# Optimization experiments

Hardware: AMD Instinct MI355X
Metric: run time of the kernel (lower is better)

The kernel has to match this reference:

```python
import jax, jax.numpy as jnp
import numpy as np

N_NODES = 100000
N_EDGES = 1000000
IN_DIM = 128
HID = 128
OUT_DIM = 40


def setup_inputs() -> dict:
    key = jax.random.key(0)
    ks = jax.random.split(key, 16)
    x = jax.random.normal(ks[0], (N_NODES, IN_DIM), dtype=jnp.float32)
    edge_index = jax.random.randint(ks[1], (2, N_EDGES), 0, N_NODES, dtype=jnp.int64)
    s = 0.05
    # GAT layer 1 (in->hid, heads=1, concat=True)
    W1 = jax.random.normal(ks[2], (HID, IN_DIM), jnp.float32) * s
    b1 = jnp.zeros((HID,), jnp.float32)
    att1 = jax.random.normal(ks[3], (1, 2 * HID), jnp.float32) * s
    bias1 = jnp.zeros((HID,), jnp.float32)
    # GAT layer 2 (hid->hid)
    W2 = jax.random.normal(ks[4], (HID, HID), jnp.float32) * s
    b2 = jnp.zeros((HID,), jnp.float32)
    att2 = jax.random.normal(ks[5], (1, 2 * HID), jnp.float32) * s
    bias2 = jnp.zeros((HID,), jnp.float32)
    # post_mp: Linear(hid,hid) -> Dropout -> Linear(hid,out)
    Wp1 = jax.random.normal(ks[6], (HID, HID), jnp.float32) * s
    bp1 = jnp.zeros((HID,), jnp.float32)
    Wp2 = jax.random.normal(ks[7], (OUT_DIM, HID), jnp.float32) * s
    bp2 = jnp.zeros((OUT_DIM,), jnp.float32)
    return dict(x=x, edge_index=edge_index, W1=W1, b1=b1, att1=att1, bias1=bias1,
                W2=W2, b2=b2, att2=att2, bias2=bias2,
                Wp1=Wp1, bp1=bp1, Wp2=Wp2, bp2=bp2)


def gat_layer(x, src, dst, W, b, att, bias, n_nodes):
    # x: [N, Fin] -> h: [N, C] (heads=1, concat=True)
    h = x @ W.T + b
    C = h.shape[1]
    att_i, att_j = att[0, :C], att[0, C:]  # split: first half pairs with x_i (dst), second with x_j (src)
    # per-node scalar projections, then gather per edge (avoids [E,2C] concat)
    e = (h @ att_i)[dst] + (h @ att_j)[src]  # [E]
    e = jnp.where(e > 0, e, 0.2 * e)  # leaky_relu(0.2)
    # segment softmax over destination nodes
    m = jax.ops.segment_max(e, dst, num_segments=n_nodes)
    ex = jnp.exp(e - m[dst])
    denom = jax.ops.segment_sum(ex, dst, num_segments=n_nodes)
    alpha = ex / denom[dst]
    out = jax.ops.segment_sum(h[src] * alpha[:, None], dst, num_segments=n_nodes)
    return out + bias


def reference(x, edge_index, W1, b1, att1, bias1, W2, b2, att2, bias2, Wp1, bp1, Wp2, bp2):
    src, dst = edge_index[0], edge_index[1]
    n = x.shape[0]
    h = jax.nn.relu(gat_layer(x, src, dst, W1, b1, att1, bias1, n))  # dropout p=0 -> identity
    h = jax.nn.relu(gat_layer(h, src, dst, W2, b2, att2, bias2, n))
    y = (h @ Wp1.T + bp1) @ Wp2.T + bp2  # post_mp (eval: dropout identity)
    return jax.nn.log_softmax(y, axis=1)
```

## Files before the change

kernel.cpp:

```cpp
#include <hip/hip_runtime.h>

#define N_NODES 100000
#define N_EDGES 1000000
#define HID 128
#define OUT_DIM 40
#define CSR_W 64
#define CUR_STRIDE 16
#define GEMM_TILES 1563
#define G2_TILES 782
#define PROJ_TILES 1563
#define EDGE_BLK 977
#define WC_BLK 21

typedef __attribute__((ext_vector_type(8))) short bf16x8;
typedef __attribute__((ext_vector_type(4))) float f32x4;

__device__ inline unsigned short f2bf(float f) {
    unsigned u = __float_as_uint(f);
    u += 0x7fffu + ((u >> 16) & 1u);
    return (unsigned short)(u >> 16);
}
__device__ inline float bf2f(unsigned short u) {
    return __uint_as_float(((unsigned)u) << 16);
}

__device__ inline float4 ld4(const float* p) { return *(const float4*)p; }
__device__ inline float4 ld4(const unsigned short* p) {
    ushort4 u = *(const ushort4*)p;
    return make_float4(bf2f(u.x), bf2f(u.y), bf2f(u.z), bf2f(u.w));
}

__global__ __launch_bounds__(256) void zero_kernel(float4* __restrict__ p, int n4) {
    int i = blockIdx.x * 256 + threadIdx.x;
    int stride = gridDim.x * 256;
    float4 z = make_float4(0.f, 0.f, 0.f, 0.f);
    for (; i < n4; i += stride) p[i] = z;
}

#define LDA 136
template<typename AT>
__device__ __forceinline__ void gemm_tile_body(
    int tile, const AT* __restrict__ A, const float* __restrict__ W,
    const float* __restrict__ out_bias, const float* __restrict__ in_bias,
    int relu_in, const float* __restrict__ att,
    unsigned short* __restrict__ Cb, float* __restrict__ hi, float* __restrict__ hj,
    int n_rows, unsigned short* As, unsigned short* Ws)
{
    const int t = threadIdx.x;
    const int row0 = tile * 64;

    for (int i = 0; i < 8; i++) {
        int lin = t + i * 256;
        int r = lin >> 5;
        int k = (lin & 31) * 4;
        int gr = row0 + r;
        float4 av = make_float4(0.f, 0.f, 0.f, 0.f);
        if (gr < n_rows) av = ld4(A + (size_t)gr * HID + k);
        if (in_bias) {
            av.x += in_bias[k + 0]; av.y += in_bias[k + 1];
            av.z += in_bias[k + 2]; av.w += in_bias[k + 3];
            if (relu_in) {
                av.x = fmaxf(av.x, 0.f); av.y = fmaxf(av.y, 0.f);
                av.z = fmaxf(av.z, 0.f); av.w = fmaxf(av.w, 0.f);
            }
        }
        ushort4 bv;
        bv.x = f2bf(av.x); bv.y = f2bf(av.y); bv.z = f2bf(av.z); bv.w = f2bf(av.w);
        *(ushort4*)(&As[r * LDA + k]) = bv;
    }
    for (int i = 0; i < 16; i++) {
        int lin = t + i * 256;
        int r = lin >> 5;
        int k = (lin & 31) * 4;
        float4 wv = *(const float4*)(W + (size_t)r * HID + k);
        ushort4 bv;
        bv.x = f2bf(wv.x); bv.y = f2bf(wv.y); bv.z = f2bf(wv.z); bv.w = f2bf(wv.w);
        *(ushort4*)(&Ws[r * LDA + k]) = bv;
    }
    __syncthreads();

    const int wave = t >> 6, lane = t & 63;
    const int lrow = lane & 15, quad = lane >> 4;
    const int wrow = wave * 16;

    f32x4 acc[8];
    #pragma unroll
    for (int ni = 0; ni < 8; ni++) acc[ni] = (f32x4){0.f, 0.f, 0.f, 0.f};

    #pragma unroll
    for (int ks = 0; ks < 4; ks++) {
        const int kb = ks * 32 + quad * 8;
        bf16x8 af = *(bf16x8*)(&As[(wrow + lrow) * LDA + kb]);
        #pragma unroll
        for (int ni = 0; ni < 8; ni++) {
            bf16x8 bfr = *(bf16x8*)(&Ws[(ni * 16 + lrow) * LDA + kb]);
            acc[ni] = __builtin_amdgcn_mfma_f32_16x16x32_bf16(af, bfr, acc[ni], 0, 0, 0);
        }
    }

    float pi[4] = {0.f, 0.f, 0.f, 0.f}, pj[4] = {0.f, 0.f, 0.f, 0.f};
    const int rbase = row0 + wrow + quad * 4;
    #pragma unroll
    for (int ni = 0; ni < 8; ni++) {
        const int col = ni * 16 + lrow;
        const float bo = out_bias[col];
        const float ai = att[col], aj = att[HID + col];
        #pragma unroll
        for (int r = 0; r < 4; r++) {
            float v = acc[ni][r] + bo;
            int gr = rbase + r;
            if (gr < n_rows) Cb[(size_t)gr * HID + col] = f2bf(v);
            pi[r] = fmaf(v, ai, pi[r]);
            pj[r] = fmaf(v, aj, pj[r]);
        }
    }
    #pragma unroll
    for (int o = 1; o < 16; o <<= 1) {
        #pragma unroll
        for (int r = 0; r < 4; r++) {
            pi[r] += __shfl_xor(pi[r], o);
            pj[r] += __shfl_xor(pj[r], o);
        }
    }
    if (lrow == 0) {
        #pragma unroll
        for (int r = 0; r < 4; r++) {
            int gr = rbase + r;
            if (gr < n_rows) { hi[gr] = pi[r]; hj[gr] = pj[r]; }
        }
    }
}

__global__ __launch_bounds__(256) void combined_prep(
    const float* __restrict__ x, const float* __restrict__ W1,
    const float* __restrict__ b1, const float* __restrict__ att1,
    const float* __restrict__ Wp1, const float* __restrict__ bp1,
    const float* __restrict__ Wp2, const float* __restrict__ bp2,
    const int* __restrict__ src, const int* __restrict__ dst,
    unsigned* __restrict__ cursor, int* __restrict__ csr,
    unsigned short* __restrict__ hbuf, float* __restrict__ hi, float* __restrict__ hj,
    float* __restrict__ Wc, float* __restrict__ bc)
{
    __shared__ unsigned short As[64 * LDA];
    __shared__ unsigned short Ws[128 * LDA];
    const int b = blockIdx.x, g = b >> 3, r = b & 7;

    if (r < 3) {
        const int eid = g * 3 + r;
        if (eid >= EDGE_BLK) return;
        int e = eid * 1024 + threadIdx.x;
        #pragma unroll
        for (int j = 0; j < 4; j++, e += 256) {
            if (e < N_EDGES) {
                int d = dst[e], s = src[e];
                unsigned p = atomicAdd(&cursor[d << 4], 1u);
                if (p < CSR_W) __builtin_nontemporal_store(s, &csr[(d << 6) + p]);
            }
        }
        return;
    }
    const int oid = g * 5 + (r - 3);
    if (oid < WC_BLK) {
        int t = oid * 256 + threadIdx.x;
        if (t < OUT_DIM * HID) {
            int o = t >> 7, k = t & 127;
            float s = 0.f;
            for (int j = 0; j < HID; j++) s = fmaf(Wp2[o * HID + j], Wp1[j * HID + k], s);
            Wc[t] = s;
        } else if (t < OUT_DIM * HID + OUT_DIM) {
            int o = t - OUT_DIM * HID;
            float s = bp2[o];
            for (int j = 0; j < HID; j++) s = fmaf(Wp2[o * HID + j], bp1[j], s);
            bc[o] = s;
        }
        return;
    }
    const int tile = oid - WC_BLK;
    if (tile >= GEMM_TILES) return;
    gemm_tile_body<float>(tile, x, W1, b1, nullptr, 0, att1, hbuf, hi, hj, N_NODES, As, Ws);
}

__global__ __launch_bounds__(256) void gemm_mfma_b128(
    const unsigned short* __restrict__ A, const float* __restrict__ W,
    const float* __restrict__ out_bias, const float* __restrict__ in_bias,
    const float* __restrict__ att,
    unsigned short* __restrict__ Cb, float* __restrict__ hi, float* __restrict__ hj,
    int n_rows)
{
    __shared__ unsigned short As[128 * LDA];
    __shared__ unsigned short Ws[128 * LDA];
    const int t = threadIdx.x;
    const int row0 = blockIdx.x * 128;

    for (int i = 0; i < 16; i++) {
        int lin = t + i * 256;
        int r = lin >> 5;
        int k = (lin & 31) * 4;
        int gr = row0 + r;
        float4 av = make_float4(0.f, 0.f, 0.f, 0.f);
        if (gr < n_rows) av = ld4(A + (size_t)gr * HID + k);
        av.x = fmaxf(av.x + in_bias[k + 0], 0.f);
        av.y = fmaxf(av.y + in_bias[k + 1], 0.f);
        av.z = fmaxf(av.z + in_bias[k + 2], 0.f);
        av.w = fmaxf(av.w + in_bias[k + 3], 0.f);
        ushort4 bv;
        bv.x = f2bf(av.x); bv.y = f2bf(av.y); bv.z = f2bf(av.z); bv.w = f2bf(av.w);
        *(ushort4*)(&As[r * LDA + k]) = bv;
    }
    for (int i = 0; i < 16; i++) {
        int lin = t + i * 256;
        int r = lin >> 5;
        int k = (lin & 31) * 4;
        float4 wv = *(const float4*)(W + (size_t)r * HID + k);
        ushort4 bv;
        bv.x = f2bf(wv.x); bv.y = f2bf(wv.y); bv.z = f2bf(wv.z); bv.w = f2bf(wv.w);
        *(ushort4*)(&Ws[r * LDA + k]) = bv;
    }
    __syncthreads();

    const int wave = t >> 6, lane = t & 63;
    const int lrow = lane & 15, quad = lane >> 4;

    f32x4 acc[2][8];
    #pragma unroll
    for (int mt = 0; mt < 2; mt++)
        #pragma unroll
        for (int ni = 0; ni < 8; ni++) acc[mt][ni] = (f32x4){0.f, 0.f, 0.f, 0.f};

    #pragma unroll
    for (int ks = 0; ks < 4; ks++) {
        const int kb = ks * 32 + quad * 8;
        bf16x8 af0 = *(bf16x8*)(&As[(wave * 32 + lrow) * LDA + kb]);
        bf16x8 af1 = *(bf16x8*)(&As[(wave * 32 + 16 + lrow) * LDA + kb]);
        #pragma unroll
        for (int ni = 0; ni < 8; ni++) {
            bf16x8 bfr = *(bf16x8*)(&Ws[(ni * 16 + lrow) * LDA + kb]);
            acc[0][ni] = __builtin_amdgcn_mfma_f32_16x16x32_bf16(af0, bfr, acc[0][ni], 0, 0, 0);
            acc[1][ni] = __builtin_amdgcn_mfma_f32_16x16x32_bf16(af1, bfr, acc[1][ni], 0, 0, 0);
        }
    }

    #pragma unroll
    for (int mt = 0; mt < 2; mt++) {
        float pi[4] = {0.f, 0.f, 0.f, 0.f}, pj[4] = {0.f, 0.f, 0.f, 0.f};
        const int rbase = row0 + wave * 32 + mt * 16 + quad * 4;
        #pragma unroll
        for (int ni = 0; ni < 8; ni++) {
            const int col = ni * 16 + lrow;
            const float bo = out_bias[col];
            const float ai = att[col], aj = att[HID + col];
            #pragma unroll
            for (int r = 0; r < 4; r++) {
                float v = acc[mt][ni][r] + bo;
                int gr = rbase + r;
                if (gr < n_rows) Cb[(size_t)gr * HID + col] = f2bf(v);
                pi[r] = fmaf(v, ai, pi[r]);
                pj[r] = fmaf(v, aj, pj[r]);
            }
        }
        #pragma unroll
        for (int o = 1; o < 16; o <<= 1) {
            #pragma unroll
            for (int r = 0; r < 4; r++) {
                pi[r] += __shfl_xor(pi[r], o);
                pj[r] += __shfl_xor(pj[r], o);
            }
        }
        if (lrow == 0) {
            #pragma unroll
            for (int r = 0; r < 4; r++) {
                int gr = rbase + r;
                if (gr < n_rows) { hi[gr] = pi[r]; hj[gr] = pj[r]; }
            }
        }
    }
}

__global__ __launch_bounds__(256) void fused_gat(
    const unsigned* __restrict__ cursor, const int* __restrict__ csr,
    const unsigned short* __restrict__ hb,
    const float* __restrict__ hi, const float* __restrict__ hj,
    unsigned short* __restrict__ out)
{
    const int wave = threadIdx.x >> 6;
    const int lane = threadIdx.x & 63;
    const int d = blockIdx.x * 4 + wave;
    if (d >= N_NODES) return;
    unsigned deg = cursor[d << 4];
    if (deg > CSR_W) deg = CSR_W;
    const int cnt = (int)deg;
    const float hid = hi[d];
    const int base = d << 6;

    int sv = 0;
    float ev = -INFINITY;
    if (lane < cnt) {
        sv = csr[base + lane];
        float e = hid + hj[sv];
        ev = e > 0.f ? e : 0.2f * e;
    }
    float m = ev;
    #pragma unroll
    for (int o = 32; o; o >>= 1) m = fmaxf(m, __shfl_xor(m, o));
    const float exv = (lane < cnt) ? __expf(ev - m) : 0.f;
    float denom = exv;
    #pragma unroll
    for (int o = 32; o; o >>= 1) denom += __shfl_xor(denom, o);

    float accx = 0.f, accy = 0.f;
    const int co = lane * 2;
    int i = 0;
    for (; i + 4 <= cnt; i += 4) {
        const int s0 = __shfl(sv, i),     s1 = __shfl(sv, i + 1);
        const int s2 = __shfl(sv, i + 2), s3 = __shfl(sv, i + 3);
        const float w0 = __shfl(exv, i),     w1 = __shfl(exv, i + 1);
        const float w2 = __shfl(exv, i + 2), w3 = __shfl(exv, i + 3);
        const ushort2 u0 = *(const ushort2*)(hb + (size_t)s0 * HID + co);
        const ushort2 u1 = *(const ushort2*)(hb + (size_t)s1 * HID + co);
        const ushort2 u2 = *(const ushort2*)(hb + (size_t)s2 * HID + co);
        const ushort2 u3 = *(const ushort2*)(hb + (size_t)s3 * HID + co);
        accx = fmaf(w0, bf2f(u0.x), accx); accy = fmaf(w0, bf2f(u0.y), accy);
        accx = fmaf(w1, bf2f(u1.x), accx); accy = fmaf(w1, bf2f(u1.y), accy);
        accx = fmaf(w2, bf2f(u2.x), accx); accy = fmaf(w2, bf2f(u2.y), accy);
        accx = fmaf(w3, bf2f(u3.x), accx); accy = fmaf(w3, bf2f(u3.y), accy);
    }
    for (; i < cnt; i++) {
        const int s = __shfl(sv, i);
        const float w = __shfl(exv, i);
        const ushort2 u = *(const ushort2*)(hb + (size_t)s * HID + co);
        accx = fmaf(w, bf2f(u.x), accx);
        accy = fmaf(w, bf2f(u.y), accy);
    }
    const float inv = cnt ? 1.f / denom : 0.f;
    ushort2 o2;
    o2.x = f2bf(accx * inv);
    o2.y = f2bf(accy * inv);
    *(ushort2*)(out + (size_t)d * HID + co) = o2;
}

__global__ __launch_bounds__(256) void final_proj_mfma(
    const unsigned short* __restrict__ agg, const float* __restrict__ bias2,
    const float* __restrict__ Wc, const float* __restrict__ bc,
    float* __restrict__ out)
{
    __shared__ unsigned short As[64 * LDA];
    __shared__ unsigned short Ws[48 * LDA];
    const int t = threadIdx.x;
    const int node0 = blockIdx.x * 64;

    for (int i = 0; i < 5; i++) {
        int lin = t + i * 256;
        int r = lin >> 5;
        int k = (lin & 31) * 4;
        float4 wv = *(const float4*)(Wc + (size_t)r * HID + k);
        ushort4 bv;
        bv.x = f2bf(wv.x); bv.y = f2bf(wv.y); bv.z = f2bf(wv.z); bv.w = f2bf(wv.w);
        *(ushort4*)(&Ws[r * LDA + k]) = bv;
    }
    {
        int r = 40 + (t >> 5);
        int k = (t & 31) * 4;
        ushort4 z; z.x = 0; z.y = 0; z.z = 0; z.w = 0;
        *(ushort4*)(&Ws[r * LDA + k]) = z;
    }
    for (int i = 0; i < 8; i++) {
        int lin = t + i * 256;
        int r = lin >> 5;
        int k = (lin & 31) * 4;
        int gr = node0 + r;
        float4 v = make_float4(0.f, 0.f, 0.f, 0.f);
        if (gr < N_NODES) v = ld4(agg + (size_t)gr * HID + k);
        v.x = fmaxf(v.x + bias2[k + 0], 0.f);
        v.y = fmaxf(v.y + bias2[k + 1], 0.f);
        v.z = fmaxf(v.z + bias2[k + 2], 0.f);
        v.w = fmaxf(v.w + bias2[k + 3], 0.f);
        ushort4 bv;
        bv.x = f2bf(v.x); bv.y = f2bf(v.y); bv.z = f2bf(v.z); bv.w = f2bf(v.w);
        *(ushort4*)(&As[r * LDA + k]) = bv;
    }
    __syncthreads();

    const int wave = t >> 6, lane = t & 63;
    const int lrow = lane & 15, quad = lane >> 4;
    const int wrow = wave * 16;

    f32x4 acc[3];
    #pragma unroll
    for (int nt = 0; nt < 3; nt++) acc[nt] = (f32x4){0.f, 0.f, 0.f, 0.f};

    #pragma unroll
    for (int ks = 0; ks < 4; ks++) {
        const int kb = ks * 32 + quad * 8;
        bf16x8 af = *(bf16x8*)(&As[(wrow + lrow) * LDA + kb]);
        #pragma unroll
        for (int nt = 0; nt < 3; nt++) {
            bf16x8 bfr = *(bf16x8*)(&Ws[(nt * 16 + lrow) * LDA + kb]);
            acc[nt] = __builtin_amdgcn_mfma_f32_16x16x32_bf16(af, bfr, acc[nt], 0, 0, 0);
        }
    }

    int cols[3]; float bcv[3]; bool valid[3];
    #pragma unroll
    for (int nt = 0; nt < 3; nt++) {
        cols[nt] = nt * 16 + lrow;
        valid[nt] = cols[nt] < OUT_DIM;
        bcv[nt] = valid[nt] ? bc[cols[nt]] : 0.f;
    }
    const int rbase = node0 + wrow + quad * 4;
    #pragma unroll
    for (int r = 0; r < 4; r++) {
        float v[3];
        float mx = -INFINITY;
        #pragma unroll
        for (int nt = 0; nt < 3; nt++) {
            v[nt] = acc[nt][r] + bcv[nt];
            if (valid[nt]) mx = fmaxf(mx, v[nt]);
        }
        #pragma unroll
        for (int o = 1; o < 16; o <<= 1) mx = fmaxf(mx, __shfl_xor(mx, o));
        float s = 0.f;
        #pragma unroll
        for (int nt = 0; nt < 3; nt++)
            if (valid[nt]) s += __expf(v[nt] - mx);
        #pragma unroll
        for (int o = 1; o < 16; o <<= 1) s += __shfl_xor(s, o);
        const float lse = mx + __logf(s);
        const int node = rbase + r;
        if (node < N_NODES) {
            #pragma unroll
            for (int nt = 0; nt < 3; nt++)
                if (valid[nt]) out[(size_t)node * OUT_DIM + cols[nt]] = v[nt] - lse;
        }
    }
}

extern "C" void kernel_launch(void* const* d_in, const int* in_sizes, int n_in,
                              void* d_out, int out_size, void* d_ws, size_t ws_size,
                              hipStream_t stream)
{
    const float* x     = (const float*)d_in[0];
    const int*   ei    = (const int*)d_in[1];
    const float* W1    = (const float*)d_in[2];
    const float* b1    = (const float*)d_in[3];
    const float* att1  = (const float*)d_in[4];
    const float* bias1 = (const float*)d_in[5];
    const float* W2    = (const float*)d_in[6];
    const float* b2    = (const float*)d_in[7];
    const float* att2  = (const float*)d_in[8];
    const float* bias2 = (const float*)d_in[9];
    const float* Wp1   = (const float*)d_in[10];
    const float* bp1   = (const float*)d_in[11];
    const float* Wp2   = (const float*)d_in[12];
    const float* bp2   = (const float*)d_in[13];
    float* out = (float*)d_out;

    const int* src = ei;
    const int* dst = ei + N_EDGES;

    char* ws = (char*)d_ws;
    unsigned short* hbuf = (unsigned short*)ws;
    unsigned short* aggb = hbuf + (size_t)N_NODES * HID;
    float* hi      = (float*)(aggb + (size_t)N_NODES * HID);
    float* hj      = hi + N_NODES;
    unsigned* cursor = (unsigned*)(hj + N_NODES);
    int* csr       = (int*)(cursor + (size_t)N_NODES * CUR_STRIDE);
    float* Wc      = (float*)(csr + (size_t)N_NODES * CSR_W);
    float* bc      = Wc + OUT_DIM * HID;

    const int prep_blocks = 326 * 8;

    zero_kernel<<<512, 256, 0, stream>>>((float4*)cursor, N_NODES * CUR_STRIDE / 4);

    combined_prep<<<prep_blocks, 256, 0, stream>>>(
        x, W1, b1, att1, Wp1, bp1, Wp2, bp2, src, dst,
        cursor, csr, hbuf, hi, hj, Wc, bc);

    fused_gat<<<N_NODES / 4, 256, 0, stream>>>(cursor, csr, hbuf, hi, hj, aggb);

    gemm_mfma_b128<<<G2_TILES, 256, 0, stream>>>(aggb, W2, b2, bias1, att2, hbuf, hi, hj, N_NODES);
    fused_gat<<<N_NODES / 4, 256, 0, stream>>>(cursor, csr, hbuf, hi, hj, aggb);

    final_proj_mfma<<<PROJ_TILES, 256, 0, stream>>>(aggb, bias2, Wc, bc, out);
}
```

Before: 313.3 us.

## Store node features as per-row scaled FP8 to halve gather traffic

The GEMM epilogues now quantize the transformed node features to FP8 (e4m3) with a per-row absmax scale instead of bf16. The scale is packed alongside the hj attention term as a float2. The GAT aggregation gathers 2 bytes per lane instead of 4 and folds the row scale into the softmax weight. This roughly halves the random-gather bandwidth in both aggregation passes, at the cost of lower feature precision and a possible accuracy-tolerance risk.

```diff
diff --git a/kernel.cpp b/kernel.cpp
--- a/kernel.cpp
+++ b/kernel.cpp
@@ -14,6 +14,7 @@
 
 typedef __attribute__((ext_vector_type(8))) short bf16x8;
 typedef __attribute__((ext_vector_type(4))) float f32x4;
+typedef __attribute__((ext_vector_type(2))) float f32x2;
 
 __device__ inline unsigned short f2bf(float f) {
     unsigned u = __float_as_uint(f);
@@ -22,6 +23,46 @@
 }
 __device__ inline float bf2f(unsigned short u) {
     return __uint_as_float(((unsigned)u) << 16);
+}
+
+#if __has_builtin(__builtin_amdgcn_cvt_pk_f32_fp8) && __has_builtin(__builtin_amdgcn_cvt_pk_fp8_f32)
+#define HAVE_HW_FP8 1
+#endif
+
+__device__ inline f32x2 fp8x2_to_f32(unsigned short u) {
+#ifdef HAVE_HW_FP8
+    return __builtin_amdgcn_cvt_pk_f32_fp8((int)(unsigned)u, false);
+#else
+    f32x2 r;
+    unsigned v0 = u & 0xFF, v1 = (u >> 8) & 0xFF;
+    unsigned m0 = v0 & 0x7F, m1 = v1 & 0x7F;
+    float a0 = (m0 >= 8) ? __uint_as_float((m0 << 20) + 0x3C000000) : (float)m0 * (1.f/512.f);
+    float a1 = (m1 >= 8) ? __uint_as_float((m1 << 20) + 0x3C000000) : (float)m1 * (1.f/512.f);
+    r.x = (v0 & 0x80) ? -a0 : a0;
+    r.y = (v1 & 0x80) ? -a1 : a1;
+    return r;
+#endif
+}
+
+__device__ inline unsigned char f32_to_fp8(float f) {
+#ifdef HAVE_HW_FP8
+    return (unsigned char)(__builtin_amdgcn_cvt_pk_fp8_f32(f, 0.f, 0u, false) & 0xFF);
+#else
+    float a = fabsf(f);
+    unsigned s = (__float_as_uint(f) >> 31) << 7;
+    if (a >= 448.f) return (unsigned char)(s | 0x7E);
+    if (a < 0.015625f) {
+        int q = (int)rintf(a * 512.f);
+        return (unsigned char)(s | q);
+    }
+    unsigned u = __float_as_uint(a);
+    u += 0x7FFFFu + ((u >> 20) & 1u);
+    int be = (int)(u >> 23) - 120;
+    unsigned m = (u >> 20) & 7;
+    if (be >= 16) return (unsigned char)(s | 0x7E);
+    if (be <= 0) { int q = (int)rintf(a * 512.f); return (unsigned char)(s | q); }
+    return (unsigned char)(s | (be << 3) | m);
+#endif
 }
 
 __device__ inline float4 ld4(const float* p) { return *(const float4*)p; }
@@ -43,7 +84,7 @@
     int tile, const AT* __restrict__ A, const float* __restrict__ W,
     const float* __restrict__ out_bias, const float* __restrict__ in_bias,
     int relu_in, const float* __restrict__ att,
-    unsigned short* __restrict__ Cb, float* __restrict__ hi, float* __restrict__ hj,
+    unsigned char* __restrict__ Cb8, float* __restrict__ hi, float2* __restrict__ hjsc,
     int n_rows, unsigned short* As, unsigned short* Ws)
 {
     const int t = threadIdx.x;
@@ -99,6 +140,7 @@
     }
 
     float pi[4] = {0.f, 0.f, 0.f, 0.f}, pj[4] = {0.f, 0.f, 0.f, 0.f};
+    float amax[4] = {0.f, 0.f, 0.f, 0.f};
     const int rbase = row0 + wrow + quad * 4;
     #pragma unroll
     for (int ni = 0; ni < 8; ni++) {
@@ -108,8 +150,7 @@
         #pragma unroll
         for (int r = 0; r < 4; r++) {
             float v = acc[ni][r] + bo;
-            int gr = rbase + r;
-            if (gr < n_rows) Cb[(size_t)gr * HID + col] = f2bf(v);
+            amax[r] = fmaxf(amax[r], fabsf(v));
             pi[r] = fmaf(v, ai, pi[r]);
             pj[r] = fmaf(v, aj, pj[r]);
         }
@@ -118,15 +159,34 @@
     for (int o = 1; o < 16; o <<= 1) {
         #pragma unroll
         for (int r = 0; r < 4; r++) {
+            amax[r] = fmaxf(amax[r], __shfl_xor(amax[r], o));
             pi[r] += __shfl_xor(pi[r], o);
             pj[r] += __shfl_xor(pj[r], o);
         }
     }
-    if (lrow == 0) {
+    float inv[4], scl[4];
+    #pragma unroll
+    for (int r = 0; r < 4; r++) {
+        float a = fmaxf(amax[r], 1e-20f);
+        scl[r] = a * (1.f / 448.f);
+        inv[r] = 448.f / a;
+    }
+    #pragma unroll
+    for (int ni = 0; ni < 8; ni++) {
+        const int col = ni * 16 + lrow;
+        const float bo = out_bias[col];
         #pragma unroll
         for (int r = 0; r < 4; r++) {
             int gr = rbase + r;
-            if (gr < n_rows) { hi[gr] = pi[r]; hj[gr] = pj[r]; }
+            if (gr < n_rows)
+                Cb8[(size_t)gr * HID + col] = f32_to_fp8((acc[ni][r] + bo) * inv[r]);
+        }
+    }
+    if (lrow == 0) {
+        #pragma unroll
+        for (int r = 0; r < 4; r++) {
+            int gr = rbase + r;
+            if (gr < n_rows) { hi[gr] = pi[r]; hjsc[gr] = make_float2(pj[r], scl[r]); }
         }
     }
 }
@@ -138,7 +198,7 @@
     const float* __restrict__ Wp2, const float* __restrict__ bp2,
     const int* __restrict__ src, const int* __restrict__ dst,
     unsigned* __restrict__ cursor, int* __restrict__ csr,
-    unsigned short* __restrict__ hbuf, float* __restrict__ hi, float* __restrict__ hj,
+    unsigned char* __restrict__ hb8, float* __restrict__ hi, float2* __restrict__ hjsc,
     float* __restrict__ Wc, float* __restrict__ bc)
 {
     __shared__ unsigned short As[64 * LDA];
@@ -177,14 +237,14 @@
     }
     const int tile = oid - WC_BLK;
     if (tile >= GEMM_TILES) return;
-    gemm_tile_body<float>(tile, x, W1, b1, nullptr, 0, att1, hbuf, hi, hj, N_NODES, As, Ws);
+    gemm_tile_body<float>(tile, x, W1, b1, nullptr, 0, att1, hb8, hi, hjsc, N_NODES, As, Ws);
 }
 
 __global__ __launch_bounds__(256) void gemm_mfma_b128(
     const unsigned short* __restrict__ A, const float* __restrict__ W,
     const float* __restrict__ out_bias, const float* __restrict__ in_bias,
     const float* __restrict__ att,
-    unsigned short* __restrict__ Cb, float* __restrict__ hi, float* __restrict__ hj,
+    unsigned char* __restrict__ Cb8, float* __restrict__ hi, float2* __restrict__ hjsc,
     int n_rows)
 {
     __shared__ unsigned short As[128 * LDA];
@@ -243,6 +303,7 @@
     #pragma unroll
     for (int mt = 0; mt < 2; mt++) {
         float pi[4] = {0.f, 0.f, 0.f, 0.f}, pj[4] = {0.f, 0.f, 0.f, 0.f};
+        float amax[4] = {0.f, 0.f, 0.f, 0.f};
         const int rbase = row0 + wave * 32 + mt * 16 + quad * 4;
         #pragma unroll
         for (int ni = 0; ni < 8; ni++) {
@@ -252,8 +313,7 @@
             #pragma unroll
             for (int r = 0; r < 4; r++) {
                 float v = acc[mt][ni][r] + bo;
-                int gr = rbase + r;
-                if (gr < n_rows) Cb[(size_t)gr * HID + col] = f2bf(v);
+                amax[r] = fmaxf(amax[r], fabsf(v));
                 pi[r] = fmaf(v, ai, pi[r]);
                 pj[r] = fmaf(v, aj, pj[r]);
             }
@@ -262,15 +322,34 @@
         for (int o = 1; o < 16; o <<= 1) {
             #pragma unroll
             for (int r = 0; r < 4; r++) {
+                amax[r] = fmaxf(amax[r], __shfl_xor(amax[r], o));
                 pi[r] += __shfl_xor(pi[r], o);
                 pj[r] += __shfl_xor(pj[r], o);
+            }
+        }
+        float inv[4], scl[4];
+        #pragma unroll
+        for (int r = 0; r < 4; r++) {
+            float a = fmaxf(amax[r], 1e-20f);
+            scl[r] = a * (1.f / 448.f);
+            inv[r] = 448.f / a;
+        }
+        #pragma unroll
+        for (int ni = 0; ni < 8; ni++) {
+            const int col = ni * 16 + lrow;
+            const float bo = out_bias[col];
+            #pragma unroll
+            for (int r = 0; r < 4; r++) {
+                int gr = rbase + r;
+                if (gr < n_rows)
+                    Cb8[(size_t)gr * HID + col] = f32_to_fp8((acc[mt][ni][r] + bo) * inv[r]);
             }
         }
         if (lrow == 0) {
             #pragma unroll
             for (int r = 0; r < 4; r++) {
                 int gr = rbase + r;
-                if (gr < n_rows) { hi[gr] = pi[r]; hj[gr] = pj[r]; }
+                if (gr < n_rows) { hi[gr] = pi[r]; hjsc[gr] = make_float2(pj[r], scl[r]); }
             }
         }
     }
@@ -278,8 +357,8 @@
 
 __global__ __launch_bounds__(256) void fused_gat(
     const unsigned* __restrict__ cursor, const int* __restrict__ csr,
-    const unsigned short* __restrict__ hb,
-    const float* __restrict__ hi, const float* __restrict__ hj,
+    const unsigned char* __restrict__ hb8,
+    const float* __restrict__ hi, const float2* __restrict__ hjsc,
     unsigned short* __restrict__ out)
 {
     const int wave = threadIdx.x >> 6;
@@ -293,11 +372,13 @@
     const int base = d << 6;
 
     int sv = 0;
-    float ev = -INFINITY;
+    float ev = -INFINITY, esc = 0.f;
     if (lane < cnt) {
         sv = csr[base + lane];
-        float e = hid + hj[sv];
+        float2 gg = hjsc[sv];
+        float e = hid + gg.x;
         ev = e > 0.f ? e : 0.2f * e;
+        esc = gg.y;
     }
     float m = ev;
     #pragma unroll
@@ -306,6 +387,7 @@
     float denom = exv;
     #pragma unroll
     for (int o = 32; o; o >>= 1) denom += __shfl_xor(denom, o);
+    const float wv = exv * esc;
 
     float accx = 0.f, accy = 0.f;
     const int co = lane * 2;
@@ -313,23 +395,28 @@
     for (; i + 4 <= cnt; i += 4) {
         const int s0 = __shfl(sv, i),     s1 = __shfl(sv, i + 1);
         const int s2 = __shfl(sv, i + 2), s3 = __shfl(sv, i + 3);
-        const float w0 = __shfl(exv, i),     w1 = __shfl(exv, i + 1);
-        const float w2 = __shfl(exv, i + 2), w3 = __shfl(exv, i + 3);
-        const ushort2 u0 = *(const ushort2*)(hb + (size_t)s0 * HID + co);
-        const ushort2 u1 = *(const ushort2*)(hb + (size_t)s1 * HID + co);
-        const ushort2 u2 = *(const ushort2*)(hb + (size_t)s2 * HID + co);
-        const ushort2 u3 = *(const ushort2*)(hb + (size_t)s3 * HID + co);
-        accx = fmaf(w0, bf2f(u0.x), accx); accy = fmaf(w0, bf2f(u0.y), accy);
-        accx = fmaf(w1, bf2f(u1.x), accx); accy = fmaf(w1, bf2f(u1.y), accy);
-        accx = fmaf(w2, bf2f(u2.x), accx); accy = fmaf(w2, bf2f(u2.y), accy);
-        accx = fmaf(w3, bf2f(u3.x), accx); accy = fmaf(w3, bf2f(u3.y), accy);
+        const float w0 = __shfl(wv, i),     w1 = __shfl(wv, i + 1);
+        const float w2 = __shfl(wv, i + 2), w3 = __shfl(wv, i + 3);
+        const unsigned short u0 = *(const unsigned short*)(hb8 + (size_t)s0 * HID + co);
+        const unsigned short u1 = *(const unsigned short*)(hb8 + (size_t)s1 * HID + co);
+        const unsigned short u2 = *(const unsigned short*)(hb8 + (size_t)s2 * HID + co);
+        const unsigned short u3 = *(const unsigned short*)(hb8 + (size_t)s3 * HID + co);
+        const f32x2 f0 = fp8x2_to_f32(u0);
+        const f32x2 f1 = fp8x2_to_f32(u1);
+        const f32x2 f2 = fp8x2_to_f32(u2);
+        const f32x2 f3 = fp8x2_to_f32(u3);
+        accx = fmaf(w0, f0.x, accx); accy = fmaf(w0, f0.y, accy);
+        accx = fmaf(w1, f1.x, accx); accy = fmaf(w1, f1.y, accy);
+        accx = fmaf(w2, f2.x, accx); accy = fmaf(w2, f2.y, accy);
+        accx = fmaf(w3, f3.x, accx); accy = fmaf(w3, f3.y, accy);
     }
     for (; i < cnt; i++) {
         const int s = __shfl(sv, i);
-        const float w = __shfl(exv, i);
-        const ushort2 u = *(const ushort2*)(hb + (size_t)s * HID + co);
-        accx = fmaf(w, bf2f(u.x), accx);
-        accy = fmaf(w, bf2f(u.y), accy);
+        const float w = __shfl(wv, i);
+        const unsigned short u = *(const unsigned short*)(hb8 + (size_t)s * HID + co);
+        const f32x2 f = fp8x2_to_f32(u);
+        accx = fmaf(w, f.x, accx);
+        accy = fmaf(w, f.y, accy);
     }
     const float inv = cnt ? 1.f / denom : 0.f;
     ushort2 o2;
@@ -458,11 +545,11 @@
     const int* dst = ei + N_EDGES;
 
     char* ws = (char*)d_ws;
-    unsigned short* hbuf = (unsigned short*)ws;
-    unsigned short* aggb = hbuf + (size_t)N_NODES * HID;
+    unsigned char* hb8   = (unsigned char*)ws;
+    unsigned short* aggb = (unsigned short*)(ws + (size_t)N_NODES * HID);
     float* hi      = (float*)(aggb + (size_t)N_NODES * HID);
-    float* hj      = hi + N_NODES;
-    unsigned* cursor = (unsigned*)(hj + N_NODES);
+    float2* hjsc   = (float2*)(hi + N_NODES);
+    unsigned* cursor = (unsigned*)(hjsc + N_NODES);
     int* csr       = (int*)(cursor + (size_t)N_NODES * CUR_STRIDE);
     float* Wc      = (float*)(csr + (size_t)N_NODES * CSR_W);
     float* bc      = Wc + OUT_DIM * HID;
@@ -473,12 +560,12 @@
 
     combined_prep<<<prep_blocks, 256, 0, stream>>>(
         x, W1, b1, att1, Wp1, bp1, Wp2, bp2, src, dst,
-        cursor, csr, hbuf, hi, hj, Wc, bc);
-
-    fused_gat<<<N_NODES / 4, 256, 0, stream>>>(cursor, csr, hbuf, hi, hj, aggb);
-
-    gemm_mfma_b128<<<G2_TILES, 256, 0, stream>>>(aggb, W2, b2, bias1, att2, hbuf, hi, hj, N_NODES);
-    fused_gat<<<N_NODES / 4, 256, 0, stream>>>(cursor, csr, hbuf, hi, hj, aggb);
+        cursor, csr, hb8, hi, hjsc, Wc, bc);
+
+    fused_gat<<<N_NODES / 4, 256, 0, stream>>>(cursor, csr, hb8, hi, hjsc, aggb);
+
+    gemm_mfma_b128<<<G2_TILES, 256, 0, stream>>>(aggb, W2, b2, bias1, att2, hb8, hi, hjsc, N_NODES);
+    fused_gat<<<N_NODES / 4, 256, 0, stream>>>(cursor, csr, hb8, hi, hjsc, aggb);
 
     final_proj_mfma<<<PROJ_TILES, 256, 0, stream>>>(aggb, bias2, Wc, bc, out);
 }
```

Result: slower. 319.8 us (+2.1%).
